# Optimization experiments

Hardware: AMD Instinct MI355X
Metric: run time of the kernel (lower is better)

Reference implementation:

```python
import jax, jax.numpy as jnp
import numpy as np

VOCAB, D, E, I, L, B, T = 32000, 1024, 8, 2048, 2, 4, 2048
LN_EPS = 1e-5


def setup_inputs() -> dict:
    key = jax.random.key(0)
    ks = jax.random.split(key, 10)
    return {
        "x": jax.random.randint(ks[0], (B, T), 0, VOCAB),
        "emb": jax.random.normal(ks[1], (VOCAB, D), jnp.float32) * 0.02,
        "ln_g": jnp.ones((L, D), jnp.float32),
        "ln_b": jnp.zeros((L, D), jnp.float32),
        "gate_w": jax.random.normal(ks[2], (L, D, E), jnp.float32) * 0.02,
        "gate_b": jnp.zeros((L, E), jnp.float32),
        "w1": jax.random.normal(ks[3], (L, E, D, I), jnp.float32) * 0.02,
        "w2": jax.random.normal(ks[4], (L, E, I, D), jnp.float32) * 0.02,
        "head_w": jax.random.normal(ks[5], (D, VOCAB), jnp.float32) * 0.02,
        "head_b": jnp.zeros((VOCAB,), jnp.float32),
    }


def _layer_norm(h, g, b):
    mu = jnp.mean(h, axis=-1, keepdims=True)
    var = jnp.mean(jnp.square(h - mu), axis=-1, keepdims=True)
    return (h - mu) * jax.lax.rsqrt(var + LN_EPS) * g + b


def reference(x, emb, ln_g, ln_b, gate_w, gate_b, w1, w2, head_w, head_b):
    h = emb[x]  # [B,T,D]
    experts_all = []
    for l in range(ln_g.shape[0]):  # small fixed layer loop
        xn = _layer_norm(h, ln_g[l], ln_b[l])
        gating_logits = xn @ gate_w[l] + gate_b[l]          # [B,T,E]
        rw = jax.nn.softmax(gating_logits, axis=-1)
        e = jnp.einsum('btc,eci->btei', xn, w1[l])           # [B,T,E,I]
        e = jax.nn.gelu(e, approximate=False)                # torch F.gelu default = erf
        eo = jnp.einsum('btei,eic->btec', e, w2[l])          # [B,T,E,D]
        agg = jnp.einsum('btec,bte->btc', eo, rw)
        h = h + agg
        experts_all.append(eo)
    logits = h @ head_w + head_b                             # [B,T,VOCAB]
    return logits, jnp.stack(experts_all)                    # [L,B,T,E,D]
```

## Files before the change

kernel.cpp:

```cpp
#include <hip/hip_runtime.h>
#include <hip/hip_bf16.h>
#include <stdint.h>

#define NTOK 8192
#define DM   1024
#define NE   8
#define DI   2048
#define NL   2
#define NV   32000

typedef __attribute__((ext_vector_type(8))) __bf16 bf16x8;
typedef __attribute__((ext_vector_type(4))) float  f32x4;
typedef __attribute__((ext_vector_type(4))) uint32_t u32x4;
typedef unsigned short u16;

__device__ __forceinline__ u16 f2bf(float f) {
  uint32_t u = __builtin_bit_cast(uint32_t, f);
  return (u16)((u + 0x7fffu + ((u >> 16) & 1u)) >> 16);
}

__device__ __forceinline__ void nts_f32x4(float* p, f32x4 v) {
  asm volatile("global_store_dwordx4 %0, %1, off sc0 sc1 nt"
               :: "v"(p), "v"(v) : "memory");
}
__device__ __forceinline__ void nts_b128(u16* p, u32x4 v) {
  asm volatile("global_store_dwordx4 %0, %1, off sc0 sc1 nt"
               :: "v"(p), "v"(v) : "memory");
}

__device__ __forceinline__ void gload_lds16(const u16* g, void* l) {
  __builtin_amdgcn_global_load_lds(
      (const __attribute__((address_space(1))) void*)g,
      (__attribute__((address_space(3))) void*)l, 16, 0, 0);
}

__device__ __forceinline__ int xcd_swz(int orig, int nwg) {
  const int x = orig & 7, i = orig >> 3;
  const int q = nwg >> 3, r = nwg & 7;
  return (x < r ? x * (q + 1) : r * (q + 1) + (x - r) * q) + i;
}

template <int EPI>
__global__ __launch_bounds__(512, 1) void k_gemm256(
    const u16* __restrict__ A0, const u16* __restrict__ W0,
    void* __restrict__ O0, const float* __restrict__ bias,
    int K, int mBlks, int nBlks,
    size_t aStride, size_t wStride, size_t oStride, int ldOut) {
  extern __shared__ char lds[];
  const int logical = xcd_swz(blockIdx.x, gridDim.x);
  const int perE = mBlks * nBlks;
  const int e    = logical / perE;
  const int rem  = logical - e * perE;
  const int mb   = rem / nBlks;
  const int nb   = rem - mb * nBlks;
  const int rowBase = mb * 256;
  const int colBase = nb * 256;
  const u16* A = A0 + (size_t)e * aStride;
  const u16* W = W0 + (size_t)e * wStride;

  const int t = threadIdx.x, lane = t & 63, wave = t >> 6;
  const int wm = wave >> 2, wn = wave & 3;
  const int fr = lane & 15, kg = lane >> 4;

  const u16* gA[2]; const u16* gB[2]; int loA[2], loB[2];
#pragma unroll
  for (int i = 0; i < 2; ++i) {
    const int c = t + 512 * i, row = c >> 2;
    const int gs = (c & 3) ^ ((row >> 2) & 3);
    gA[i] = A + (size_t)(rowBase + row) * K + gs * 8;
    gB[i] = W + (size_t)(colBase + row) * K + gs * 8;
    loA[i] = c * 16;
    loB[i] = 16384 + c * 16;
  }

  auto stage = [&](int g) {
    char* dst = lds + (g & 3) * 32768;
#pragma unroll
    for (int i = 0; i < 2; ++i) {
      gload_lds16(gA[i] + (size_t)g * 32, dst + loA[i]);
      gload_lds16(gB[i] + (size_t)g * 32, dst + loB[i]);
    }
  };

  const int swzo = (kg ^ ((fr >> 2) & 3)) * 16;
  const int aOff = (wm * 128 + fr) * 64 + swzo;
  const int bOff = 16384 + (wn * 64 + fr) * 64 + swzo;

  f32x4 acc[8][4] = {};
  const int NG = K >> 5;

  auto khalf = [&](int g, bool doStage) {
    __builtin_amdgcn_s_barrier();
    asm volatile("" ::: "memory");
    const char* base = lds + (g & 3) * 32768;
    bf16x8 af[8], bv[4];
#pragma unroll
    for (int mi = 0; mi < 8; ++mi) af[mi] = *(const bf16x8*)(base + aOff + mi * 1024);
#pragma unroll
    for (int ni = 0; ni < 4; ++ni) bv[ni] = *(const bf16x8*)(base + bOff + ni * 1024);
    if (doStage) stage(g + 3);
    __builtin_amdgcn_s_setprio(1);
#pragma unroll
    for (int mi = 0; mi < 8; ++mi)
#pragma unroll
      for (int ni = 0; ni < 4; ++ni)
        acc[mi][ni] = __builtin_amdgcn_mfma_f32_16x16x32_bf16(
            af[mi], bv[ni], acc[mi][ni], 0, 0, 0);
    __builtin_amdgcn_s_setprio(0);
  };

  stage(0); stage(1); stage(2);

#pragma unroll 1
  for (int g = 0; g < NG - 3; ++g) {
    asm volatile("s_waitcnt vmcnt(8)" ::: "memory");
    khalf(g, true);
  }
  asm volatile("s_waitcnt vmcnt(8)" ::: "memory");
  khalf(NG - 3, false);
  asm volatile("s_waitcnt vmcnt(4)" ::: "memory");
  khalf(NG - 2, false);
  asm volatile("s_waitcnt vmcnt(0)" ::: "memory");
  khalf(NG - 1, false);

  float* ep = (float*)lds;
  const int colL0 = wn * 64 + fr;
  __syncthreads();
#pragma unroll 1
  for (int p = 0; p < 2; ++p) {
    if (wm == p) {
#pragma unroll
      for (int mi = 0; mi < 8; ++mi)
#pragma unroll
        for (int ni = 0; ni < 4; ++ni) {
          const int rl = mi * 16 + (kg << 2);
          const int cl = colL0 + ni * 16;
#pragma unroll
          for (int j = 0; j < 4; ++j)
            ep[(rl + j) * 256 + cl] = acc[mi][ni][j];
        }
    }
    __syncthreads();
    if (EPI == 1) {
      u16* O = (u16*)O0 + (size_t)e * oStride;
#pragma unroll
      for (int ii = 0; ii < 8; ++ii) {
        const int chunk = t + 512 * ii;
        const int rl = chunk >> 5;
        const int cl = (chunk & 31) << 3;
        const f32x4 v0 = *(const f32x4*)(ep + rl * 256 + cl);
        const f32x4 v1 = *(const f32x4*)(ep + rl * 256 + cl + 4);
        float gv[8];
#pragma unroll
        for (int j = 0; j < 4; ++j) {
          gv[j]     = 0.5f * v0[j] * (1.0f + erff(v0[j] * 0.70710678118654752f));
          gv[4 + j] = 0.5f * v1[j] * (1.0f + erff(v1[j] * 0.70710678118654752f));
        }
        u32x4 pk;
        pk.x = (uint32_t)f2bf(gv[0]) | ((uint32_t)f2bf(gv[1]) << 16);
        pk.y = (uint32_t)f2bf(gv[2]) | ((uint32_t)f2bf(gv[3]) << 16);
        pk.z = (uint32_t)f2bf(gv[4]) | ((uint32_t)f2bf(gv[5]) << 16);
        pk.w = (uint32_t)f2bf(gv[6]) | ((uint32_t)f2bf(gv[7]) << 16);
        const int row = rowBase + p * 128 + rl;
        nts_b128(&O[(size_t)row * ldOut + colBase + cl], pk);
      }
    } else {
      float* O = (float*)O0 + (EPI == 2 ? (size_t)e * oStride : (size_t)0);
#pragma unroll
      for (int ii = 0; ii < 16; ++ii) {
        const int chunk = t + 512 * ii;
        const int rl = chunk >> 6;
        const int cl = (chunk & 63) << 2;
        f32x4 v = *(const f32x4*)(ep + rl * 256 + cl);
        if (EPI == 0) v += *(const f32x4*)(bias + colBase + cl);
        const int row = rowBase + p * 128 + rl;
        nts_f32x4(&O[(size_t)row * ldOut + colBase + cl], v);
      }
    }
    __syncthreads();
  }
}

__global__ void k_transcvt(const float* __restrict__ in, u16* __restrict__ out,
                           int R, int C) {
  const size_t bo = (size_t)blockIdx.z * R * C;
  in += bo; out += bo;
  __shared__ u16 tile[32][33];
  const int tx = threadIdx.x, ty = threadIdx.y;
  const int r0 = blockIdx.y << 5, c0 = blockIdx.x << 5;
#pragma unroll
  for (int j = 0; j < 4; ++j) {
    const int r = r0 + ty + j * 8;
    tile[ty + j * 8][tx] = f2bf(in[(size_t)r * C + c0 + tx]);
  }
  __syncthreads();
#pragma unroll
  for (int j = 0; j < 4; ++j) {
    const int c = c0 + ty + j * 8;
    out[(size_t)c * R + r0 + tx] = tile[tx][ty + j * 8];
  }
}

__global__ void k_gather(const int* __restrict__ x, const float* __restrict__ emb,
                         float* __restrict__ h) {
  const int n = blockIdx.x, t = threadIdx.x;
  const int id = x[n];
  ((float4*)(h + (size_t)n * DM))[t] = ((const float4*)(emb + (size_t)id * DM))[t];
}

__global__ void k_lngate(const float* __restrict__ h, const float* __restrict__ g,
                         const float* __restrict__ b, const float* __restrict__ gw,
                         const float* __restrict__ gb, u16* __restrict__ xnb,
                         float* __restrict__ rw) {
  const int n = blockIdx.x, t = threadIdx.x;
  const int wave = t >> 6, lane = t & 63;
  const float4 v = ((const float4*)(h + (size_t)n * DM))[t];
  float s = v.x + v.y + v.z + v.w;
  float q = v.x * v.x + v.y * v.y + v.z * v.z + v.w * v.w;
#pragma unroll
  for (int o = 32; o; o >>= 1) { s += __shfl_down(s, o, 64); q += __shfl_down(q, o, 64); }
  __shared__ float red[8];
  if (lane == 0) { red[wave] = s; red[wave + 4] = q; }
  __syncthreads();
  s = red[0] + red[1] + red[2] + red[3];
  q = red[4] + red[5] + red[6] + red[7];
  const float mu = s * (1.0f / DM);
  const float var = q * (1.0f / DM) - mu * mu;
  const float rs = rsqrtf(var + 1e-5f);
  const float4 gg = ((const float4*)g)[t];
  const float4 bb = ((const float4*)b)[t];
  float xv[4];
  xv[0] = (v.x - mu) * rs * gg.x + bb.x;
  xv[1] = (v.y - mu) * rs * gg.y + bb.y;
  xv[2] = (v.z - mu) * rs * gg.z + bb.z;
  xv[3] = (v.w - mu) * rs * gg.w + bb.w;
  ushort4 o4;
  o4.x = f2bf(xv[0]); o4.y = f2bf(xv[1]); o4.z = f2bf(xv[2]); o4.w = f2bf(xv[3]);
  ((ushort4*)(xnb + (size_t)n * DM))[t] = o4;
  float p[8];
#pragma unroll
  for (int e = 0; e < 8; ++e) p[e] = 0.0f;
  const float* gwp = gw + (size_t)t * 32;
#pragma unroll
  for (int j = 0; j < 4; ++j)
#pragma unroll
    for (int e = 0; e < 8; ++e) p[e] += xv[j] * gwp[j * 8 + e];
#pragma unroll
  for (int e = 0; e < 8; ++e)
#pragma unroll
    for (int o = 32; o; o >>= 1) p[e] += __shfl_down(p[e], o, 64);
  __shared__ float pr[4][8];
  if (lane == 0) {
#pragma unroll
    for (int e = 0; e < 8; ++e) pr[wave][e] = p[e];
  }
  __syncthreads();
  if (t == 0) {
    float lg[8], m = -1e30f;
#pragma unroll
    for (int e = 0; e < 8; ++e) {
      lg[e] = pr[0][e] + pr[1][e] + pr[2][e] + pr[3][e] + gb[e];
      m = fmaxf(m, lg[e]);
    }
    float ss = 0.0f;
#pragma unroll
    for (int e = 0; e < 8; ++e) { lg[e] = expf(lg[e] - m); ss += lg[e]; }
    const float inv = 1.0f / ss;
#pragma unroll
    for (int e = 0; e < 8; ++e) rw[(size_t)n * NE + e] = lg[e] * inv;
  }
}

__global__ void k_agg(float* __restrict__ h, u16* __restrict__ hbf,
                      const float* __restrict__ eo, const float* __restrict__ rw) {
  const int n = blockIdx.x, t = threadIdx.x;
  float w[8];
#pragma unroll
  for (int e = 0; e < 8; ++e) w[e] = rw[(size_t)n * NE + e];
  const f32x4* eo4 = (const f32x4*)(eo + (size_t)n * NE * DM);
  f32x4 a = ((f32x4*)(h + (size_t)n * DM))[t];
#pragma unroll
  for (int e = 0; e < 8; ++e) {
    const f32x4 xv = __builtin_nontemporal_load(&eo4[e * (DM / 4) + t]);
    a += w[e] * xv;
  }
  ((f32x4*)(h + (size_t)n * DM))[t] = a;
  ushort4 o4;
  o4.x = f2bf(a.x); o4.y = f2bf(a.y); o4.z = f2bf(a.z); o4.w = f2bf(a.w);
  ((ushort4*)(hbf + (size_t)n * DM))[t] = o4;
}

extern "C" void kernel_launch(void* const* d_in, const int* in_sizes, int n_in,
                              void* d_out, int out_size, void* d_ws, size_t ws_size,
                              hipStream_t stream) {
  const int*   x      = (const int*)d_in[0];
  const float* emb    = (const float*)d_in[1];
  const float* ln_g   = (const float*)d_in[2];
  const float* ln_b   = (const float*)d_in[3];
  const float* gate_w = (const float*)d_in[4];
  const float* gate_b = (const float*)d_in[5];
  const float* w1     = (const float*)d_in[6];
  const float* w2     = (const float*)d_in[7];
  const float* head_w = (const float*)d_in[8];
  const float* head_b = (const float*)d_in[9];

  float* logits  = (float*)d_out;
  float* experts = logits + (size_t)NTOK * NV;

  char* p = (char*)d_ws;
  auto carve = [&](size_t bytes) -> void* {
    void* r = (void*)p; p += (bytes + 255) & ~(size_t)255; return r;
  };
  float* h   = (float*)carve((size_t)NTOK * DM * 4);
  u16*   hbf = (u16*)  carve((size_t)NTOK * DM * 2);
  u16*   xnb = (u16*)  carve((size_t)NTOK * DM * 2);
  float* rw  = (float*)carve((size_t)NTOK * NE * 4);
  u16*   w1t = (u16*)  carve((size_t)NE * DM * DI * 2);
  u16*   w2t = (u16*)  carve((size_t)NE * DM * DI * 2);
  u16*   hwt = (u16*)  carve((size_t)NV * DM * 2);
  const size_t fixed = (size_t)(p - (char*)d_ws);
  const size_t eactOne = (size_t)NTOK * DI * 2;
  const bool batched = ws_size >= fixed + eactOne * NE;
  u16* eact = (u16*)carve(batched ? eactOne * NE : eactOne);

  const int LDSB = 131072;
  (void)hipFuncSetAttribute((const void*)k_gemm256<0>,
                            hipFuncAttributeMaxDynamicSharedMemorySize, LDSB);
  (void)hipFuncSetAttribute((const void*)k_gemm256<1>,
                            hipFuncAttributeMaxDynamicSharedMemorySize, LDSB);
  (void)hipFuncSetAttribute((const void*)k_gemm256<2>,
                            hipFuncAttributeMaxDynamicSharedMemorySize, LDSB);

  const int MB = NTOK / 256;

  k_gather<<<dim3(NTOK), dim3(256), 0, stream>>>(x, emb, h);

  for (int l = 0; l < NL; ++l) {
    k_lngate<<<dim3(NTOK), dim3(256), 0, stream>>>(
        h, ln_g + (size_t)l * DM, ln_b + (size_t)l * DM,
        gate_w + (size_t)l * DM * NE, gate_b + (size_t)l * NE, xnb, rw);
    k_transcvt<<<dim3(DI / 32, DM / 32, NE), dim3(32, 8), 0, stream>>>(
        w1 + (size_t)l * NE * DM * DI, w1t, DM, DI);
    k_transcvt<<<dim3(DM / 32, DI / 32, NE), dim3(32, 8), 0, stream>>>(
        w2 + (size_t)l * NE * DM * DI, w2t, DI, DM);
    float* expertsL = experts + (size_t)l * NTOK * NE * DM;
    if (batched) {
      k_gemm256<1><<<dim3(NE * MB * (DI / 256)), dim3(512), LDSB, stream>>>(
          xnb, w1t, eact, nullptr, DM, MB, DI / 256,
          (size_t)0, (size_t)DM * DI, (size_t)NTOK * DI, DI);
      k_gemm256<2><<<dim3(NE * MB * (DM / 256)), dim3(512), LDSB, stream>>>(
          eact, w2t, expertsL, nullptr, DI, MB, DM / 256,
          (size_t)NTOK * DI, (size_t)DM * DI, (size_t)DM, NE * DM);
    } else {
      for (int e = 0; e < NE; ++e) {
        k_gemm256<1><<<dim3(MB * (DI / 256)), dim3(512), LDSB, stream>>>(
            xnb, w1t + (size_t)e * DM * DI, eact, nullptr, DM, MB, DI / 256,
            (size_t)0, (size_t)0, (size_t)0, DI);
        k_gemm256<2><<<dim3(MB * (DM / 256)), dim3(512), LDSB, stream>>>(
            eact, w2t + (size_t)e * DM * DI, expertsL + (size_t)e * DM, nullptr,
            DI, MB, DM / 256, (size_t)0, (size_t)0, (size_t)0, NE * DM);
      }
    }
    k_agg<<<dim3(NTOK), dim3(256), 0, stream>>>(h, hbf, expertsL, rw);
  }

  k_transcvt<<<dim3(NV / 32, DM / 32, 1), dim3(32, 8), 0, stream>>>(head_w, hwt, DM, NV);
  k_gemm256<0><<<dim3(MB * (NV / 256)), dim3(512), LDSB, stream>>>(
      hbf, hwt, logits, head_b, DM, MB, NV / 256,
      (size_t)0, (size_t)0, (size_t)0, NV);
}
```

Before: 2.172 ms.

## Split GEMM k-step into two half-phases interleaving LDS reads, prefetch and MFMA

Restructures the main GEMM loop so each k-step runs as two halves. Each half loads half the A fragments, issues half of the next-stage global-to-LDS prefetch, and then runs 16 MFMAs, with barriers and sched_barriers between halves. The vmcnt wait moves inside the step so memory issue spreads across the compute. This lowers register pressure from the fragments and aims for finer-grained overlap, at the cost of extra barriers per k-step.

```diff
diff --git a/kernel.cpp b/kernel.cpp
--- a/kernel.cpp
+++ b/kernel.cpp
@@ -73,7 +73,7 @@
     loB[i] = 16384 + c * 16;
   }
 
-  auto stage = [&](int g) {
+  auto stageFull = [&](int g) {
     char* dst = lds + (g & 3) * 32768;
 #pragma unroll
     for (int i = 0; i < 2; ++i) {
@@ -89,39 +89,64 @@
   f32x4 acc[8][4] = {};
   const int NG = K >> 5;
 
-  auto khalf = [&](int g, bool doStage) {
+  auto khalf = [&](int g, bool doStage, int tail) {
+    const char* base = lds + (g & 3) * 32768;
+    char* dstN = lds + ((g + 3) & 3) * 32768;
+    bf16x8 a0[4], a1[4], bv[4];
+#pragma unroll
+    for (int mi = 0; mi < 4; ++mi) a0[mi] = *(const bf16x8*)(base + aOff + mi * 1024);
+#pragma unroll
+    for (int ni = 0; ni < 4; ++ni) bv[ni] = *(const bf16x8*)(base + bOff + ni * 1024);
+    if (doStage) {
+      gload_lds16(gA[0] + (size_t)(g + 3) * 32, dstN + loA[0]);
+      gload_lds16(gB[0] + (size_t)(g + 3) * 32, dstN + loB[0]);
+    }
+    __builtin_amdgcn_s_barrier();
+    asm volatile("s_waitcnt lgkmcnt(0)" ::: "memory");
+    __builtin_amdgcn_sched_barrier(0);
+    __builtin_amdgcn_s_setprio(1);
+#pragma unroll
+    for (int mi = 0; mi < 4; ++mi)
+#pragma unroll
+      for (int ni = 0; ni < 4; ++ni)
+        acc[mi][ni] = __builtin_amdgcn_mfma_f32_16x16x32_bf16(
+            a0[mi], bv[ni], acc[mi][ni], 0, 0, 0);
+    __builtin_amdgcn_s_setprio(0);
     __builtin_amdgcn_s_barrier();
     asm volatile("" ::: "memory");
-    const char* base = lds + (g & 3) * 32768;
-    bf16x8 af[8], bv[4];
-#pragma unroll
-    for (int mi = 0; mi < 8; ++mi) af[mi] = *(const bf16x8*)(base + aOff + mi * 1024);
-#pragma unroll
-    for (int ni = 0; ni < 4; ++ni) bv[ni] = *(const bf16x8*)(base + bOff + ni * 1024);
-    if (doStage) stage(g + 3);
+#pragma unroll
+    for (int mi = 0; mi < 4; ++mi) a1[mi] = *(const bf16x8*)(base + aOff + (4 + mi) * 1024);
+    if (doStage) {
+      gload_lds16(gA[1] + (size_t)(g + 3) * 32, dstN + loA[1]);
+      gload_lds16(gB[1] + (size_t)(g + 3) * 32, dstN + loB[1]);
+    }
+    if (tail == 8)      asm volatile("s_waitcnt vmcnt(8)" ::: "memory");
+    else if (tail == 4) asm volatile("s_waitcnt vmcnt(4)" ::: "memory");
+    else if (tail == 0) asm volatile("s_waitcnt vmcnt(0)" ::: "memory");
+    __builtin_amdgcn_s_barrier();
+    asm volatile("s_waitcnt lgkmcnt(0)" ::: "memory");
+    __builtin_amdgcn_sched_barrier(0);
     __builtin_amdgcn_s_setprio(1);
 #pragma unroll
-    for (int mi = 0; mi < 8; ++mi)
+    for (int mi = 0; mi < 4; ++mi)
 #pragma unroll
       for (int ni = 0; ni < 4; ++ni)
-        acc[mi][ni] = __builtin_amdgcn_mfma_f32_16x16x32_bf16(
-            af[mi], bv[ni], acc[mi][ni], 0, 0, 0);
+        acc[4 + mi][ni] = __builtin_amdgcn_mfma_f32_16x16x32_bf16(
+            a1[mi], bv[ni], acc[4 + mi][ni], 0, 0, 0);
     __builtin_amdgcn_s_setprio(0);
+    __builtin_amdgcn_s_barrier();
+    asm volatile("" ::: "memory");
   };
 
-  stage(0); stage(1); stage(2);
+  stageFull(0); stageFull(1); stageFull(2);
+  asm volatile("s_waitcnt vmcnt(8)" ::: "memory");
+  __builtin_amdgcn_s_barrier();
 
 #pragma unroll 1
-  for (int g = 0; g < NG - 3; ++g) {
-    asm volatile("s_waitcnt vmcnt(8)" ::: "memory");
-    khalf(g, true);
-  }
-  asm volatile("s_waitcnt vmcnt(8)" ::: "memory");
-  khalf(NG - 3, false);
-  asm volatile("s_waitcnt vmcnt(4)" ::: "memory");
-  khalf(NG - 2, false);
-  asm volatile("s_waitcnt vmcnt(0)" ::: "memory");
-  khalf(NG - 1, false);
+  for (int g = 0; g < NG - 3; ++g) khalf(g, true, 8);
+  khalf(NG - 3, false, 4);
+  khalf(NG - 2, false, 0);
+  khalf(NG - 1, false, -1);
 
   float* ep = (float*)lds;
   const int colL0 = wn * 64 + fr;
```

New measurement: 2.271 ms. 4.6% more time.
